# Performance work log

Measured on AMD Instinct MI355X. Metric: run time of the kernel, lower is better.

Reference implementation:

```python
import math
import jax, jax.numpy as jnp
import numpy as np
from jax import lax

N = 224
EPS_BN = 1e-5


def _conv(x, w, b):
    y = lax.conv_general_dilated(x, w, (1, 1), 'SAME',
                                 dimension_numbers=('NCHW', 'OIHW', 'NCHW'))
    return y + b[None, :, None, None]


def _bn(x, g, beta, m, v):
    # eval-mode BatchNorm2d with running stats
    inv = lax.rsqrt(v + EPS_BN)
    return (x - m[None, :, None, None]) * (g * inv)[None, :, None, None] + beta[None, :, None, None]


def _maxpool2(x):
    return lax.reduce_window(x, -jnp.inf, lax.max, (1, 1, 2, 2), (1, 1, 2, 2), 'VALID')


def setup_inputs() -> dict:
    key = jax.random.key(0)
    ks = jax.random.split(key, 12)
    idx = np.arange(N, dtype=np.float32)
    angles = 2.0 * math.pi * idx[None, :] * idx[:, None] / N
    inp = {
        'sequences': jax.random.normal(ks[0], (16, 8, 3, N, N), dtype=jnp.float32),
        'dft_cos': jnp.asarray(np.cos(angles), dtype=jnp.float32),
        'dft_sin': jnp.asarray(np.sin(angles), dtype=jnp.float32),
        'conv1_w': jax.random.normal(ks[1], (16, 3, 3, 3), dtype=jnp.float32) * 0.1,
        'conv1_b': jnp.zeros((16,), jnp.float32),
        'bn1_g': jnp.ones((16,), jnp.float32),
        'bn1_b': jnp.zeros((16,), jnp.float32),
        'bn1_m': jnp.zeros((16,), jnp.float32),
        'bn1_v': jnp.ones((16,), jnp.float32),
        'conv2_w': jax.random.normal(ks[2], (32, 16, 3, 3), dtype=jnp.float32) * 0.05,
        'conv2_b': jnp.zeros((32,), jnp.float32),
        'bn2_g': jnp.ones((32,), jnp.float32),
        'bn2_b': jnp.zeros((32,), jnp.float32),
        'bn2_m': jnp.zeros((32,), jnp.float32),
        'bn2_v': jnp.ones((32,), jnp.float32),
        'conv3_w': jax.random.normal(ks[3], (64, 32, 3, 3), dtype=jnp.float32) * 0.05,
        'conv3_b': jnp.zeros((64,), jnp.float32),
        'bn3_g': jnp.ones((64,), jnp.float32),
        'bn3_b': jnp.zeros((64,), jnp.float32),
        'bn3_m': jnp.zeros((64,), jnp.float32),
        'bn3_v': jnp.ones((64,), jnp.float32),
        'fc_w': jax.random.normal(ks[4], (128, 64), dtype=jnp.float32) * 0.1,
        'fc_b': jnp.zeros((128,), jnp.float32),
    }
    return inp


def reference(sequences, dft_cos, dft_sin,
              conv1_w, conv1_b, bn1_g, bn1_b, bn1_m, bn1_v,
              conv2_w, conv2_b, bn2_g, bn2_b, bn2_m, bn2_v,
              conv3_w, conv3_b, bn3_g, bn3_b, bn3_m, bn3_v,
              fc_w, fc_b):
    b, s = sequences.shape[0], sequences.shape[1]
    x = sequences[:, s // 2]  # center frames [B,3,H,W]

    # 2D DFT via dense matmul chain: X = (C - jS) x (C - jS)
    C, S = dft_cos, dft_sin
    Cx = jnp.einsum('ij,bcjk->bcik', C, x)
    Sx = jnp.einsum('ij,bcjk->bcik', S, x)
    X_real = jnp.einsum('bcij,jk->bcik', Cx, C) - jnp.einsum('bcij,jk->bcik', Sx, S)
    X_imag = -(jnp.einsum('bcij,jk->bcik', Cx, S) + jnp.einsum('bcij,jk->bcik', Sx, C))
    magnitude = jnp.sqrt(X_real ** 2 + X_imag ** 2 + 1e-08)
    spec = jnp.log(magnitude + 1e-08)
    half = N // 2
    spec = jnp.roll(spec, shift=(half, half), axis=(-2, -1))  # fftshift

    # CNN stack (eval-mode BN, dropout disabled)
    h = jax.nn.relu(_bn(_conv(spec, conv1_w, conv1_b), bn1_g, bn1_b, bn1_m, bn1_v))
    h = _maxpool2(h)
    h = jax.nn.relu(_bn(_conv(h, conv2_w, conv2_b), bn2_g, bn2_b, bn2_m, bn2_v))
    h = _maxpool2(h)
    h = jax.nn.relu(_bn(_conv(h, conv3_w, conv3_b), bn3_g, bn3_b, bn3_m, bn3_v))
    h = jnp.mean(h, axis=(2, 3))  # AdaptiveAvgPool2d((1,1)) + flatten -> [B,64]

    freq_out = jax.nn.relu(h @ fc_w.T + fc_b)  # dropout = identity in eval
    return freq_out
```

## Files before the change

kernel.cpp:

```cpp
#include <hip/hip_runtime.h>
#include <math.h>
#include <stddef.h>

#define N224 224
#define PIX 50176
#define ROWS113 25312

__global__ __launch_bounds__(64) void dft1(
    const float* __restrict__ seq, const float* __restrict__ Cm,
    const float* __restrict__ Sm, float* __restrict__ Cx, float* __restrict__ Sx)
{
  const int p = blockIdx.z;
  const int b = p / 3, ch = p % 3;
  const float* __restrict__ x = seq + ((((size_t)b * 8 + 4) * 3 + ch) * PIX);
  const int i0 = blockIdx.y * 32;
  const int k0 = blockIdx.x * 32;
  const int tid = threadIdx.x;
  const int tx = tid & 7, ty = tid >> 3;
  __shared__ float Ctt[16][36], Stt[16][36], Xt[16][36];
  float aC[4][4], aS[4][4];
#pragma unroll
  for (int a = 0; a < 4; ++a)
#pragma unroll
    for (int d = 0; d < 4; ++d) { aC[a][d] = 0.f; aS[a][d] = 0.f; }

  const int sr = tid >> 1;
  const int sk = (tid & 1) * 8;
  const int xj = tid >> 2;
  const int xk = (tid & 3) * 8;

  for (int jt = 0; jt < 14; ++jt) {
    const int j = jt * 16;
    __syncthreads();
    {
      const float4* gp = (const float4*)(x + (size_t)(j + xj) * N224 + k0 + xk);
      const float4 v0 = gp[0], v1 = gp[1];
      *(float4*)&Xt[xj][xk]     = v0;
      *(float4*)&Xt[xj][xk + 4] = v1;
    }
    {
      const float4* gc = (const float4*)(Cm + (size_t)(i0 + sr) * N224 + j + sk);
      const float4* gs = (const float4*)(Sm + (size_t)(i0 + sr) * N224 + j + sk);
      const float4 c0 = gc[0], c1 = gc[1];
      const float4 s0 = gs[0], s1 = gs[1];
      Ctt[sk+0][sr]=c0.x; Ctt[sk+1][sr]=c0.y; Ctt[sk+2][sr]=c0.z; Ctt[sk+3][sr]=c0.w;
      Ctt[sk+4][sr]=c1.x; Ctt[sk+5][sr]=c1.y; Ctt[sk+6][sr]=c1.z; Ctt[sk+7][sr]=c1.w;
      Stt[sk+0][sr]=s0.x; Stt[sk+1][sr]=s0.y; Stt[sk+2][sr]=s0.z; Stt[sk+3][sr]=s0.w;
      Stt[sk+4][sr]=s1.x; Stt[sk+5][sr]=s1.y; Stt[sk+6][sr]=s1.z; Stt[sk+7][sr]=s1.w;
    }
    __syncthreads();
#pragma unroll
    for (int jj = 0; jj < 16; ++jj) {
      const float4 cv4 = *(const float4*)&Ctt[jj][4*ty];
      const float4 sv4 = *(const float4*)&Stt[jj][4*ty];
      const float4 xv4 = *(const float4*)&Xt[jj][4*tx];
      const float cva[4] = {cv4.x, cv4.y, cv4.z, cv4.w};
      const float sva[4] = {sv4.x, sv4.y, sv4.z, sv4.w};
      const float xva[4] = {xv4.x, xv4.y, xv4.z, xv4.w};
#pragma unroll
      for (int a = 0; a < 4; ++a)
#pragma unroll
        for (int d = 0; d < 4; ++d) {
          aC[a][d] = fmaf(cva[a], xva[d], aC[a][d]);
          aS[a][d] = fmaf(sva[a], xva[d], aS[a][d]);
        }
    }
  }
  const size_t b113 = (size_t)p * ROWS113;
#pragma unroll
  for (int a = 0; a < 4; ++a) {
    const int i = i0 + 4*ty + a;
    if (i <= 112) {
      const size_t off = b113 + (size_t)i * N224 + k0 + 4*tx;
      *(float4*)&Cx[off] = make_float4(aC[a][0], aC[a][1], aC[a][2], aC[a][3]);
      *(float4*)&Sx[off] = make_float4(aS[a][0], aS[a][1], aS[a][2], aS[a][3]);
    }
  }
}

__global__ __launch_bounds__(64) void dft2(
    const float* __restrict__ Cx, const float* __restrict__ Sx,
    const float* __restrict__ Cm, const float* __restrict__ Sm,
    float* __restrict__ spec)
{
  const int p = blockIdx.z;
  const int i0 = blockIdx.y * 32;
  const int k0 = blockIdx.x * 32;
  const int tid = threadIdx.x;
  const int tx = tid & 7, ty = tid >> 3;
  const size_t b113 = (size_t)p * ROWS113;
  __shared__ float CxT[16][36], SxT[16][36], Ct[16][36], St[16][36];
  float p1[4][4], p2[4][4], p3[4][4], p4[4][4];
#pragma unroll
  for (int a = 0; a < 4; ++a)
#pragma unroll
    for (int d = 0; d < 4; ++d) { p1[a][d]=0.f; p2[a][d]=0.f; p3[a][d]=0.f; p4[a][d]=0.f; }

  const int sr = tid >> 1;
  const int sk = (tid & 1) * 8;
  const int ri = (i0 + sr > 112) ? 112 : i0 + sr;
  const int xj = tid >> 2;
  const int xk = (tid & 3) * 8;

  for (int jt = 0; jt < 14; ++jt) {
    const int j = jt * 16;
    __syncthreads();
    {
      const float4* gc = (const float4*)(Cm + (size_t)(j + xj) * N224 + k0 + xk);
      const float4* gs = (const float4*)(Sm + (size_t)(j + xj) * N224 + k0 + xk);
      const float4 c0 = gc[0], c1 = gc[1];
      const float4 s0 = gs[0], s1 = gs[1];
      *(float4*)&Ct[xj][xk]     = c0;  *(float4*)&Ct[xj][xk + 4] = c1;
      *(float4*)&St[xj][xk]     = s0;  *(float4*)&St[xj][xk + 4] = s1;
    }
    {
      const float4* gx = (const float4*)(Cx + b113 + (size_t)ri * N224 + j + sk);
      const float4* gy = (const float4*)(Sx + b113 + (size_t)ri * N224 + j + sk);
      const float4 c0 = gx[0], c1 = gx[1];
      const float4 s0 = gy[0], s1 = gy[1];
      CxT[sk+0][sr]=c0.x; CxT[sk+1][sr]=c0.y; CxT[sk+2][sr]=c0.z; CxT[sk+3][sr]=c0.w;
      CxT[sk+4][sr]=c1.x; CxT[sk+5][sr]=c1.y; CxT[sk+6][sr]=c1.z; CxT[sk+7][sr]=c1.w;
      SxT[sk+0][sr]=s0.x; SxT[sk+1][sr]=s0.y; SxT[sk+2][sr]=s0.z; SxT[sk+3][sr]=s0.w;
      SxT[sk+4][sr]=s1.x; SxT[sk+5][sr]=s1.y; SxT[sk+6][sr]=s1.z; SxT[sk+7][sr]=s1.w;
    }
    __syncthreads();
#pragma unroll
    for (int jj = 0; jj < 16; ++jj) {
      const float4 cx4 = *(const float4*)&CxT[jj][4*ty];
      const float4 sx4 = *(const float4*)&SxT[jj][4*ty];
      const float4 cc4 = *(const float4*)&Ct[jj][4*tx];
      const float4 ss4 = *(const float4*)&St[jj][4*tx];
      const float cxa[4] = {cx4.x, cx4.y, cx4.z, cx4.w};
      const float sxa[4] = {sx4.x, sx4.y, sx4.z, sx4.w};
      const float cca[4] = {cc4.x, cc4.y, cc4.z, cc4.w};
      const float ssa[4] = {ss4.x, ss4.y, ss4.z, ss4.w};
#pragma unroll
      for (int a = 0; a < 4; ++a)
#pragma unroll
        for (int d = 0; d < 4; ++d) {
          p1[a][d] = fmaf(cxa[a], cca[d], p1[a][d]);
          p2[a][d] = fmaf(sxa[a], ssa[d], p2[a][d]);
          p3[a][d] = fmaf(cxa[a], ssa[d], p3[a][d]);
          p4[a][d] = fmaf(sxa[a], cca[d], p4[a][d]);
        }
    }
  }
  const size_t sb = (size_t)p * PIX;
  const int kk0 = k0 + 4*tx;
  const int ok0 = (kk0 < 112) ? kk0 + 112 : kk0 - 112;
#pragma unroll
  for (int a = 0; a < 4; ++a) {
    const int i = i0 + 4*ty + a;
    if (i > 112) continue;
    float sp1[4], sp2[4];
#pragma unroll
    for (int d = 0; d < 4; ++d) {
      const float re = p1[a][d] - p2[a][d];
      const float im = p3[a][d] + p4[a][d];
      sp1[d] = logf(sqrtf(fmaf(re, re, fmaf(im, im, 1e-8f))) + 1e-8f);
      const float re2 = p1[a][d] + p2[a][d];
      const float im2 = p3[a][d] - p4[a][d];
      sp2[d] = logf(sqrtf(fmaf(re2, re2, fmaf(im2, im2, 1e-8f))) + 1e-8f);
    }
    const int oi = (i < 112) ? i + 112 : i - 112;
    *(float4*)&spec[sb + (size_t)oi * N224 + ok0] =
        make_float4(sp1[0], sp1[1], sp1[2], sp1[3]);
    if (i >= 1 && i <= 111)
      *(float4*)&spec[sb + (size_t)(112 - i) * N224 + ok0] =
          make_float4(sp2[0], sp2[1], sp2[2], sp2[3]);
  }
}

__global__ __launch_bounds__(256) void conv1_band(
    const float* __restrict__ spec, const float* __restrict__ w,
    const float* __restrict__ cb, const float* __restrict__ g,
    const float* __restrict__ be, const float* __restrict__ mm,
    const float* __restrict__ vv, float* __restrict__ out)
{
  const int band = blockIdx.x;
  const int b    = blockIdx.y;
  const int tid  = threadIdx.x;
  const int co   = tid & 15;
  const int q    = tid >> 4;
  const int cy0  = band * 4;
  __shared__ float in_t[3][6][228];
  __shared__ float wt[3][9][16];
  for (int i = tid; i < 3*6*224; i += 256) {
    const int x = i % 224, r = (i / 224) % 6, cc = i / 1344;
    const int y = cy0 - 1 + r;
    float v = 0.f;
    if (y >= 0 && y < 224)
      v = spec[((size_t)b*3 + cc) * PIX + (size_t)y * N224 + x];
    in_t[cc][r][x+1] = v;
  }
  if (tid < 18) { const int cc = tid / 6, r = tid % 6;
                  in_t[cc][r][0] = 0.f; in_t[cc][r][225] = 0.f; }
  for (int i = tid; i < 3*9*16; i += 256) {
    const int coi = i & 15, k = (i >> 4) % 9, cc = i / 144;
    wt[cc][k][coi] = w[coi*27 + cc*9 + k];
  }
  __syncthreads();
  float acc[4][14];
#pragma unroll
  for (int i = 0; i < 4; ++i)
#pragma unroll
    for (int jx = 0; jx < 14; ++jx) acc[i][jx] = 0.f;
  const int x0 = q * 14;
#pragma unroll
  for (int cc = 0; cc < 3; ++cc) {
    float wr[9];
#pragma unroll
    for (int k = 0; k < 9; ++k) wr[k] = wt[cc][k][co];
#pragma unroll
    for (int rr = 0; rr < 6; ++rr) {
      float xr[16];
      const float2* rp = (const float2*)(&in_t[cc][rr][x0]);
#pragma unroll
      for (int t = 0; t < 8; ++t) { const float2 v = rp[t]; xr[2*t] = v.x; xr[2*t+1] = v.y; }
#pragma unroll
      for (int crow = 0; crow < 4; ++crow) {
        const int krow = rr - crow;
        if (krow < 0 || krow > 2) continue;
#pragma unroll
        for (int xx = 0; xx < 14; ++xx) {
          acc[crow][xx] = fmaf(xr[xx  ], wr[krow*3  ], acc[crow][xx]);
          acc[crow][xx] = fmaf(xr[xx+1], wr[krow*3+1], acc[crow][xx]);
          acc[crow][xx] = fmaf(xr[xx+2], wr[krow*3+2], acc[crow][xx]);
        }
      }
    }
  }
  const float s  = g[co] * rsqrtf(vv[co] + 1e-5f);
  const float sh = be[co] - mm[co]*s;
  const float bb = cb[co];
  const int py0 = band * 2, px0 = q * 7;
#pragma unroll
  for (int pr = 0; pr < 2; ++pr)
#pragma unroll
    for (int px = 0; px < 7; ++px) {
      const float v0 = (acc[2*pr  ][2*px  ] + bb)*s + sh;
      const float v1 = (acc[2*pr  ][2*px+1] + bb)*s + sh;
      const float v2 = (acc[2*pr+1][2*px  ] + bb)*s + sh;
      const float v3 = (acc[2*pr+1][2*px+1] + bb)*s + sh;
      out[(((size_t)b*16 + co)*112 + py0+pr)*112 + px0+px] =
          fmaxf(fmaxf(fmaxf(v0, v1), fmaxf(v2, v3)), 0.f);
    }
}

__global__ __launch_bounds__(256) void conv2_band(
    const float* __restrict__ h1, const float* __restrict__ w,
    const float* __restrict__ cb, const float* __restrict__ g,
    const float* __restrict__ be, const float* __restrict__ mm,
    const float* __restrict__ vv, float* __restrict__ out)
{
  const int band = blockIdx.x;
  const int b    = blockIdx.y;
  const int tid  = threadIdx.x;
  const int co   = tid & 31;
  const int q    = tid >> 5;
  const int cy0  = band * 4;
  __shared__ float in_t[8][6][114];
  __shared__ float wt[8][9][32];
  float acc[4][14];
#pragma unroll
  for (int i = 0; i < 4; ++i)
#pragma unroll
    for (int jx = 0; jx < 14; ++jx) acc[i][jx] = 0.f;

  for (int chunk = 0; chunk < 2; ++chunk) {
    const int ci0 = chunk * 8;
    __syncthreads();
    for (int i = tid; i < 8*6*112; i += 256) {
      const int x = i % 112, r = (i / 112) % 6, cc = i / 672;
      const int y = cy0 - 1 + r;
      float v = 0.f;
      if (y >= 0 && y < 112)
        v = h1[(((size_t)b*16 + ci0+cc)*112 + y)*112 + x];
      in_t[cc][r][x+1] = v;
    }
    if (tid < 48) { const int cc = tid / 6, r = tid % 6;
                    in_t[cc][r][0] = 0.f; in_t[cc][r][113] = 0.f; }
    for (int i = tid; i < 8*9*32; i += 256) {
      const int coi = i & 31, k = (i >> 5) % 9, cc = i / 288;
      wt[cc][k][coi] = w[coi*144 + (ci0+cc)*9 + k];
    }
    __syncthreads();
    const int x0 = q * 14;
    for (int cc = 0; cc < 8; ++cc) {
      float wr[9];
#pragma unroll
      for (int k = 0; k < 9; ++k) wr[k] = wt[cc][k][co];
#pragma unroll
      for (int rr = 0; rr < 6; ++rr) {
        float xr[16];
        const float2* rp = (const float2*)(&in_t[cc][rr][x0]);
#pragma unroll
        for (int t = 0; t < 8; ++t) { const float2 v = rp[t]; xr[2*t] = v.x; xr[2*t+1] = v.y; }
#pragma unroll
        for (int crow = 0; crow < 4; ++crow) {
          const int krow = rr - crow;
          if (krow < 0 || krow > 2) continue;
#pragma unroll
          for (int x = 0; x < 14; ++x) {
            acc[crow][x] = fmaf(xr[x  ], wr[krow*3  ], acc[crow][x]);
            acc[crow][x] = fmaf(xr[x+1], wr[krow*3+1], acc[crow][x]);
            acc[crow][x] = fmaf(xr[x+2], wr[krow*3+2], acc[crow][x]);
          }
        }
      }
    }
  }
  const float s  = g[co] * rsqrtf(vv[co] + 1e-5f);
  const float sh = be[co] - mm[co]*s;
  const float bb = cb[co];
  const int py0 = band * 2, px0 = q * 7;
#pragma unroll
  for (int pr = 0; pr < 2; ++pr)
#pragma unroll
    for (int px = 0; px < 7; ++px) {
      const float v0 = (acc[2*pr  ][2*px  ] + bb)*s + sh;
      const float v1 = (acc[2*pr  ][2*px+1] + bb)*s + sh;
      const float v2 = (acc[2*pr+1][2*px  ] + bb)*s + sh;
      const float v3 = (acc[2*pr+1][2*px+1] + bb)*s + sh;
      out[(((size_t)b*32 + co)*56 + py0+pr)*56 + px0+px] =
          fmaxf(fmaxf(fmaxf(v0, v1), fmaxf(v2, v3)), 0.f);
    }
}

__global__ __launch_bounds__(256) void conv3_band(
    const float* __restrict__ h2, const float* __restrict__ w,
    const float* __restrict__ cb, const float* __restrict__ g,
    const float* __restrict__ be, const float* __restrict__ mm,
    const float* __restrict__ vv, float* __restrict__ part)
{
  const int band = blockIdx.x;
  const int b    = blockIdx.y;
  const int tid  = threadIdx.x;
  const int co   = tid & 63;
  const int q    = tid >> 6;
  const int y0   = band * 2;
  __shared__ float in_t[8][4][58];
  __shared__ float wt[8][9][64];
  __shared__ float red[4][64];
  float acc[2][14];
#pragma unroll
  for (int i = 0; i < 2; ++i)
#pragma unroll
    for (int jx = 0; jx < 14; ++jx) acc[i][jx] = 0.f;

  for (int chunk = 0; chunk < 4; ++chunk) {
    const int ci0 = chunk * 8;
    __syncthreads();
    for (int i = tid; i < 8*4*56; i += 256) {
      const int x = i % 56, r = (i / 56) % 4, cc = i / 224;
      const int y = y0 - 1 + r;
      float v = 0.f;
      if (y >= 0 && y < 56)
        v = h2[(((size_t)b*32 + ci0+cc)*56 + y)*56 + x];
      in_t[cc][r][x+1] = v;
    }
    if (tid < 32) { const int cc = tid >> 2, r = tid & 3;
                    in_t[cc][r][0] = 0.f; in_t[cc][r][57] = 0.f; }
    for (int i = tid; i < 8*9*64; i += 256) {
      const int coi = i & 63, k = (i >> 6) % 9, cc = i / 576;
      wt[cc][k][coi] = w[coi*288 + (ci0+cc)*9 + k];
    }
    __syncthreads();
    const int x0 = q * 14;
    for (int cc = 0; cc < 8; ++cc) {
      float wr[9];
#pragma unroll
      for (int k = 0; k < 9; ++k) wr[k] = wt[cc][k][co];
#pragma unroll
      for (int rr = 0; rr < 4; ++rr) {
        float xr[16];
        const float2* rp = (const float2*)(&in_t[cc][rr][x0]);
#pragma unroll
        for (int t = 0; t < 8; ++t) { const float2 v = rp[t]; xr[2*t] = v.x; xr[2*t+1] = v.y; }
#pragma unroll
        for (int orow = 0; orow < 2; ++orow) {
          const int krow = rr - orow;
          if (krow < 0 || krow > 2) continue;
#pragma unroll
          for (int x = 0; x < 14; ++x) {
            acc[orow][x] = fmaf(xr[x  ], wr[krow*3  ], acc[orow][x]);
            acc[orow][x] = fmaf(xr[x+1], wr[krow*3+1], acc[orow][x]);
            acc[orow][x] = fmaf(xr[x+2], wr[krow*3+2], acc[orow][x]);
          }
        }
      }
    }
  }
  const float s  = g[co] * rsqrtf(vv[co] + 1e-5f);
  const float sh = be[co] - mm[co]*s;
  const float bb = cb[co];
  float sum = 0.f;
#pragma unroll
  for (int orow = 0; orow < 2; ++orow)
#pragma unroll
    for (int x = 0; x < 14; ++x)
      sum += fmaxf((acc[orow][x] + bb)*s + sh, 0.f);
  red[q][co] = sum;
  __syncthreads();
  if (tid < 64)
    part[(((size_t)b*64 + co)*28) + band] =
        red[0][co] + red[1][co] + red[2][co] + red[3][co];
}

__global__ __launch_bounds__(256) void reduce_mean(
    const float* __restrict__ part, float* __restrict__ h3)
{
  const int idx = blockIdx.x * 256 + threadIdx.x;
  if (idx >= 1024) return;
  float s = 0.f;
#pragma unroll
  for (int bnd = 0; bnd < 28; ++bnd) s += part[(size_t)idx*28 + bnd];
  h3[idx] = s * (1.0f / 3136.0f);
}

__global__ __launch_bounds__(256) void fc_relu(
    const float* __restrict__ h3, const float* __restrict__ fw,
    const float* __restrict__ fb, float* __restrict__ out)
{
  const int idx = blockIdx.x * 256 + threadIdx.x;
  if (idx >= 16*128) return;
  const int o = idx % 128, b = idx / 128;
  float acc = fb[o];
#pragma unroll
  for (int c = 0; c < 64; ++c)
    acc = fmaf(h3[b*64 + c], fw[o*64 + c], acc);
  out[idx] = fmaxf(acc, 0.f);
}

extern "C" void kernel_launch(void* const* d_in, const int* in_sizes, int n_in,
                              void* d_out, int out_size, void* d_ws, size_t ws_size,
                              hipStream_t stream) {
  const float* seq  = (const float*)d_in[0];
  const float* dcos = (const float*)d_in[1];
  const float* dsin = (const float*)d_in[2];
  const float* c1w  = (const float*)d_in[3];
  const float* c1b  = (const float*)d_in[4];
  const float* b1g  = (const float*)d_in[5];
  const float* b1b  = (const float*)d_in[6];
  const float* b1m  = (const float*)d_in[7];
  const float* b1v  = (const float*)d_in[8];
  const float* c2w  = (const float*)d_in[9];
  const float* c2b  = (const float*)d_in[10];
  const float* b2g  = (const float*)d_in[11];
  const float* b2b  = (const float*)d_in[12];
  const float* b2m  = (const float*)d_in[13];
  const float* b2v  = (const float*)d_in[14];
  const float* c3w  = (const float*)d_in[15];
  const float* c3b  = (const float*)d_in[16];
  const float* b3g  = (const float*)d_in[17];
  const float* b3b  = (const float*)d_in[18];
  const float* b3m  = (const float*)d_in[19];
  const float* b3v  = (const float*)d_in[20];
  const float* fw   = (const float*)d_in[21];
  const float* fb   = (const float*)d_in[22];
  float* out = (float*)d_out;

  float* ws   = (float*)d_ws;
  float* Cx   = ws;
  float* Sx   = ws + 1214976;
  float* spec = ws + 4816896;
  float* h1   = ws;
  float* h2   = ws + 4816896;
  float* part = ws;
  float* h3   = ws + 7225344;

  dft1<<<dim3(7, 4, 48), 64, 0, stream>>>(seq, dcos, dsin, Cx, Sx);
  dft2<<<dim3(7, 4, 48), 64, 0, stream>>>(Cx, Sx, dcos, dsin, spec);
  conv1_band<<<dim3(56, 16), 256, 0, stream>>>(spec, c1w, c1b, b1g, b1b, b1m, b1v, h1);
  conv2_band<<<dim3(28, 16), 256, 0, stream>>>(h1, c2w, c2b, b2g, b2b, b2m, b2v, h2);
  conv3_band<<<dim3(28, 16), 256, 0, stream>>>(h2, c3w, c3b, b3g, b3b, b3m, b3v, part);
  reduce_mean<<<4, 256, 0, stream>>>(part, h3);
  fc_relu<<<8, 256, 0, stream>>>(h3, fw, fb, out);
}
```

Baseline: 197.9 us.

## Prefetch DFT tiles into registers, halve conv bands, fuse mean and FC

The two DFT matmul kernels now load the next k-tile from global memory into registers while the current tile is being computed, a register-level double buffer that hides load latency. Each conv kernel now handles half as many rows per block, so twice as many blocks are launched to fill the GPU better. In exchange, the overlapping halo rows are reloaded more often. The reduce-mean and FC kernels are merged into a single kernel, removing one launch.

```diff
diff --git a/kernel.cpp b/kernel.cpp
--- a/kernel.cpp
+++ b/kernel.cpp
@@ -29,26 +29,35 @@
   const int xj = tid >> 2;
   const int xk = (tid & 3) * 8;
 
+  const float* xbase = x  + (size_t)xj * N224 + k0 + xk;
+  const float* cbase = Cm + (size_t)(i0 + sr) * N224 + sk;
+  const float* sbase = Sm + (size_t)(i0 + sr) * N224 + sk;
+
+  float4 rx0 = *(const float4*)(xbase);
+  float4 rx1 = *(const float4*)(xbase + 4);
+  float4 rc0 = *(const float4*)(cbase);
+  float4 rc1 = *(const float4*)(cbase + 4);
+  float4 rs0 = *(const float4*)(sbase);
+  float4 rs1 = *(const float4*)(sbase + 4);
+
   for (int jt = 0; jt < 14; ++jt) {
-    const int j = jt * 16;
-    __syncthreads();
-    {
-      const float4* gp = (const float4*)(x + (size_t)(j + xj) * N224 + k0 + xk);
-      const float4 v0 = gp[0], v1 = gp[1];
-      *(float4*)&Xt[xj][xk]     = v0;
-      *(float4*)&Xt[xj][xk + 4] = v1;
-    }
-    {
-      const float4* gc = (const float4*)(Cm + (size_t)(i0 + sr) * N224 + j + sk);
-      const float4* gs = (const float4*)(Sm + (size_t)(i0 + sr) * N224 + j + sk);
-      const float4 c0 = gc[0], c1 = gc[1];
-      const float4 s0 = gs[0], s1 = gs[1];
-      Ctt[sk+0][sr]=c0.x; Ctt[sk+1][sr]=c0.y; Ctt[sk+2][sr]=c0.z; Ctt[sk+3][sr]=c0.w;
-      Ctt[sk+4][sr]=c1.x; Ctt[sk+5][sr]=c1.y; Ctt[sk+6][sr]=c1.z; Ctt[sk+7][sr]=c1.w;
-      Stt[sk+0][sr]=s0.x; Stt[sk+1][sr]=s0.y; Stt[sk+2][sr]=s0.z; Stt[sk+3][sr]=s0.w;
-      Stt[sk+4][sr]=s1.x; Stt[sk+5][sr]=s1.y; Stt[sk+6][sr]=s1.z; Stt[sk+7][sr]=s1.w;
-    }
-    __syncthreads();
+    __syncthreads();
+    *(float4*)&Xt[xj][xk]     = rx0;
+    *(float4*)&Xt[xj][xk + 4] = rx1;
+    Ctt[sk+0][sr]=rc0.x; Ctt[sk+1][sr]=rc0.y; Ctt[sk+2][sr]=rc0.z; Ctt[sk+3][sr]=rc0.w;
+    Ctt[sk+4][sr]=rc1.x; Ctt[sk+5][sr]=rc1.y; Ctt[sk+6][sr]=rc1.z; Ctt[sk+7][sr]=rc1.w;
+    Stt[sk+0][sr]=rs0.x; Stt[sk+1][sr]=rs0.y; Stt[sk+2][sr]=rs0.z; Stt[sk+3][sr]=rs0.w;
+    Stt[sk+4][sr]=rs1.x; Stt[sk+5][sr]=rs1.y; Stt[sk+6][sr]=rs1.z; Stt[sk+7][sr]=rs1.w;
+    __syncthreads();
+    if (jt < 13) {
+      const int j = (jt + 1) * 16;
+      rx0 = *(const float4*)(xbase + (size_t)j * N224);
+      rx1 = *(const float4*)(xbase + (size_t)j * N224 + 4);
+      rc0 = *(const float4*)(cbase + j);
+      rc1 = *(const float4*)(cbase + j + 4);
+      rs0 = *(const float4*)(sbase + j);
+      rs1 = *(const float4*)(sbase + j + 4);
+    }
 #pragma unroll
     for (int jj = 0; jj < 16; ++jj) {
       const float4 cv4 = *(const float4*)&Ctt[jj][4*ty];
@@ -102,28 +111,40 @@
   const int xj = tid >> 2;
   const int xk = (tid & 3) * 8;
 
+  const float* cxb = Cx + b113 + (size_t)ri * N224 + sk;
+  const float* sxb = Sx + b113 + (size_t)ri * N224 + sk;
+  const float* ccb = Cm + (size_t)xj * N224 + k0 + xk;
+  const float* ssb = Sm + (size_t)xj * N224 + k0 + xk;
+
+  float4 ra0 = *(const float4*)(cxb);
+  float4 ra1 = *(const float4*)(cxb + 4);
+  float4 rb0 = *(const float4*)(sxb);
+  float4 rb1 = *(const float4*)(sxb + 4);
+  float4 rc0 = *(const float4*)(ccb);
+  float4 rc1 = *(const float4*)(ccb + 4);
+  float4 rd0 = *(const float4*)(ssb);
+  float4 rd1 = *(const float4*)(ssb + 4);
+
   for (int jt = 0; jt < 14; ++jt) {
-    const int j = jt * 16;
-    __syncthreads();
-    {
-      const float4* gc = (const float4*)(Cm + (size_t)(j + xj) * N224 + k0 + xk);
-      const float4* gs = (const float4*)(Sm + (size_t)(j + xj) * N224 + k0 + xk);
-      const float4 c0 = gc[0], c1 = gc[1];
-      const float4 s0 = gs[0], s1 = gs[1];
-      *(float4*)&Ct[xj][xk]     = c0;  *(float4*)&Ct[xj][xk + 4] = c1;
-      *(float4*)&St[xj][xk]     = s0;  *(float4*)&St[xj][xk + 4] = s1;
-    }
-    {
-      const float4* gx = (const float4*)(Cx + b113 + (size_t)ri * N224 + j + sk);
-      const float4* gy = (const float4*)(Sx + b113 + (size_t)ri * N224 + j + sk);
-      const float4 c0 = gx[0], c1 = gx[1];
-      const float4 s0 = gy[0], s1 = gy[1];
-      CxT[sk+0][sr]=c0.x; CxT[sk+1][sr]=c0.y; CxT[sk+2][sr]=c0.z; CxT[sk+3][sr]=c0.w;
-      CxT[sk+4][sr]=c1.x; CxT[sk+5][sr]=c1.y; CxT[sk+6][sr]=c1.z; CxT[sk+7][sr]=c1.w;
-      SxT[sk+0][sr]=s0.x; SxT[sk+1][sr]=s0.y; SxT[sk+2][sr]=s0.z; SxT[sk+3][sr]=s0.w;
-      SxT[sk+4][sr]=s1.x; SxT[sk+5][sr]=s1.y; SxT[sk+6][sr]=s1.z; SxT[sk+7][sr]=s1.w;
-    }
-    __syncthreads();
+    __syncthreads();
+    *(float4*)&Ct[xj][xk]     = rc0;  *(float4*)&Ct[xj][xk + 4] = rc1;
+    *(float4*)&St[xj][xk]     = rd0;  *(float4*)&St[xj][xk + 4] = rd1;
+    CxT[sk+0][sr]=ra0.x; CxT[sk+1][sr]=ra0.y; CxT[sk+2][sr]=ra0.z; CxT[sk+3][sr]=ra0.w;
+    CxT[sk+4][sr]=ra1.x; CxT[sk+5][sr]=ra1.y; CxT[sk+6][sr]=ra1.z; CxT[sk+7][sr]=ra1.w;
+    SxT[sk+0][sr]=rb0.x; SxT[sk+1][sr]=rb0.y; SxT[sk+2][sr]=rb0.z; SxT[sk+3][sr]=rb0.w;
+    SxT[sk+4][sr]=rb1.x; SxT[sk+5][sr]=rb1.y; SxT[sk+6][sr]=rb1.z; SxT[sk+7][sr]=rb1.w;
+    __syncthreads();
+    if (jt < 13) {
+      const int j = (jt + 1) * 16;
+      ra0 = *(const float4*)(cxb + j);
+      ra1 = *(const float4*)(cxb + j + 4);
+      rb0 = *(const float4*)(sxb + j);
+      rb1 = *(const float4*)(sxb + j + 4);
+      rc0 = *(const float4*)(ccb + (size_t)j * N224);
+      rc1 = *(const float4*)(ccb + (size_t)j * N224 + 4);
+      rd0 = *(const float4*)(ssb + (size_t)j * N224);
+      rd1 = *(const float4*)(ssb + (size_t)j * N224 + 4);
+    }
 #pragma unroll
     for (int jj = 0; jj < 16; ++jj) {
       const float4 cx4 = *(const float4*)&CxT[jj][4*ty];
@@ -182,27 +203,27 @@
   const int tid  = threadIdx.x;
   const int co   = tid & 15;
   const int q    = tid >> 4;
-  const int cy0  = band * 4;
-  __shared__ float in_t[3][6][228];
+  const int cy0  = band * 2;
+  __shared__ float in_t[3][4][228];
   __shared__ float wt[3][9][16];
-  for (int i = tid; i < 3*6*224; i += 256) {
-    const int x = i % 224, r = (i / 224) % 6, cc = i / 1344;
+  for (int i = tid; i < 3*4*224; i += 256) {
+    const int x = i % 224, r = (i / 224) % 4, cc = i / 896;
     const int y = cy0 - 1 + r;
     float v = 0.f;
     if (y >= 0 && y < 224)
       v = spec[((size_t)b*3 + cc) * PIX + (size_t)y * N224 + x];
     in_t[cc][r][x+1] = v;
   }
-  if (tid < 18) { const int cc = tid / 6, r = tid % 6;
+  if (tid < 12) { const int cc = tid / 4, r = tid % 4;
                   in_t[cc][r][0] = 0.f; in_t[cc][r][225] = 0.f; }
   for (int i = tid; i < 3*9*16; i += 256) {
     const int coi = i & 15, k = (i >> 4) % 9, cc = i / 144;
     wt[cc][k][coi] = w[coi*27 + cc*9 + k];
   }
   __syncthreads();
-  float acc[4][14];
-#pragma unroll
-  for (int i = 0; i < 4; ++i)
+  float acc[2][14];
+#pragma unroll
+  for (int i = 0; i < 2; ++i)
 #pragma unroll
     for (int jx = 0; jx < 14; ++jx) acc[i][jx] = 0.f;
   const int x0 = q * 14;
@@ -212,13 +233,13 @@
 #pragma unroll
     for (int k = 0; k < 9; ++k) wr[k] = wt[cc][k][co];
 #pragma unroll
-    for (int rr = 0; rr < 6; ++rr) {
+    for (int rr = 0; rr < 4; ++rr) {
       float xr[16];
       const float2* rp = (const float2*)(&in_t[cc][rr][x0]);
 #pragma unroll
       for (int t = 0; t < 8; ++t) { const float2 v = rp[t]; xr[2*t] = v.x; xr[2*t+1] = v.y; }
 #pragma unroll
-      for (int crow = 0; crow < 4; ++crow) {
+      for (int crow = 0; crow < 2; ++crow) {
         const int krow = rr - crow;
         if (krow < 0 || krow > 2) continue;
 #pragma unroll
@@ -233,18 +254,16 @@
   const float s  = g[co] * rsqrtf(vv[co] + 1e-5f);
   const float sh = be[co] - mm[co]*s;
   const float bb = cb[co];
-  const int py0 = band * 2, px0 = q * 7;
-#pragma unroll
-  for (int pr = 0; pr < 2; ++pr)
-#pragma unroll
-    for (int px = 0; px < 7; ++px) {
-      const float v0 = (acc[2*pr  ][2*px  ] + bb)*s + sh;
-      const float v1 = (acc[2*pr  ][2*px+1] + bb)*s + sh;
-      const float v2 = (acc[2*pr+1][2*px  ] + bb)*s + sh;
-      const float v3 = (acc[2*pr+1][2*px+1] + bb)*s + sh;
-      out[(((size_t)b*16 + co)*112 + py0+pr)*112 + px0+px] =
-          fmaxf(fmaxf(fmaxf(v0, v1), fmaxf(v2, v3)), 0.f);
-    }
+  const int px0 = q * 7;
+#pragma unroll
+  for (int px = 0; px < 7; ++px) {
+    const float v0 = (acc[0][2*px  ] + bb)*s + sh;
+    const float v1 = (acc[0][2*px+1] + bb)*s + sh;
+    const float v2 = (acc[1][2*px  ] + bb)*s + sh;
+    const float v3 = (acc[1][2*px+1] + bb)*s + sh;
+    out[(((size_t)b*16 + co)*112 + band)*112 + px0+px] =
+        fmaxf(fmaxf(fmaxf(v0, v1), fmaxf(v2, v3)), 0.f);
+  }
 }
 
 __global__ __launch_bounds__(256) void conv2_band(
@@ -258,27 +277,27 @@
   const int tid  = threadIdx.x;
   const int co   = tid & 31;
   const int q    = tid >> 5;
-  const int cy0  = band * 4;
-  __shared__ float in_t[8][6][114];
+  const int cy0  = band * 2;
+  __shared__ float in_t[8][4][114];
   __shared__ float wt[8][9][32];
-  float acc[4][14];
-#pragma unroll
-  for (int i = 0; i < 4; ++i)
+  float acc[2][14];
+#pragma unroll
+  for (int i = 0; i < 2; ++i)
 #pragma unroll
     for (int jx = 0; jx < 14; ++jx) acc[i][jx] = 0.f;
 
   for (int chunk = 0; chunk < 2; ++chunk) {
     const int ci0 = chunk * 8;
     __syncthreads();
-    for (int i = tid; i < 8*6*112; i += 256) {
-      const int x = i % 112, r = (i / 112) % 6, cc = i / 672;
+    for (int i = tid; i < 8*4*112; i += 256) {
+      const int x = i % 112, r = (i / 112) % 4, cc = i / 448;
       const int y = cy0 - 1 + r;
       float v = 0.f;
       if (y >= 0 && y < 112)
         v = h1[(((size_t)b*16 + ci0+cc)*112 + y)*112 + x];
       in_t[cc][r][x+1] = v;
     }
-    if (tid < 48) { const int cc = tid / 6, r = tid % 6;
+    if (tid < 32) { const int cc = tid >> 2, r = tid & 3;
                     in_t[cc][r][0] = 0.f; in_t[cc][r][113] = 0.f; }
     for (int i = tid; i < 8*9*32; i += 256) {
       const int coi = i & 31, k = (i >> 5) % 9, cc = i / 288;
@@ -291,13 +310,13 @@
 #pragma unroll
       for (int k = 0; k < 9; ++k) wr[k] = wt[cc][k][co];
 #pragma unroll
-      for (int rr = 0; rr < 6; ++rr) {
+      for (int rr = 0; rr < 4; ++rr) {
         float xr[16];
         const float2* rp = (const float2*)(&in_t[cc][rr][x0]);
 #pragma unroll
         for (int t = 0; t < 8; ++t) { const float2 v = rp[t]; xr[2*t] = v.x; xr[2*t+1] = v.y; }
 #pragma unroll
-        for (int crow = 0; crow < 4; ++crow) {
+        for (int crow = 0; crow < 2; ++crow) {
           const int krow = rr - crow;
           if (krow < 0 || krow > 2) continue;
 #pragma unroll
@@ -313,18 +332,16 @@
   const float s  = g[co] * rsqrtf(vv[co] + 1e-5f);
   const float sh = be[co] - mm[co]*s;
   const float bb = cb[co];
-  const int py0 = band * 2, px0 = q * 7;
-#pragma unroll
-  for (int pr = 0; pr < 2; ++pr)
-#pragma unroll
-    for (int px = 0; px < 7; ++px) {
-      const float v0 = (acc[2*pr  ][2*px  ] + bb)*s + sh;
-      const float v1 = (acc[2*pr  ][2*px+1] + bb)*s + sh;
-      const float v2 = (acc[2*pr+1][2*px  ] + bb)*s + sh;
-      const float v3 = (acc[2*pr+1][2*px+1] + bb)*s + sh;
-      out[(((size_t)b*32 + co)*56 + py0+pr)*56 + px0+px] =
-          fmaxf(fmaxf(fmaxf(v0, v1), fmaxf(v2, v3)), 0.f);
-    }
+  const int px0 = q * 7;
+#pragma unroll
+  for (int px = 0; px < 7; ++px) {
+    const float v0 = (acc[0][2*px  ] + bb)*s + sh;
+    const float v1 = (acc[0][2*px+1] + bb)*s + sh;
+    const float v2 = (acc[1][2*px  ] + bb)*s + sh;
+    const float v3 = (acc[1][2*px+1] + bb)*s + sh;
+    out[(((size_t)b*32 + co)*56 + band)*56 + px0+px] =
+        fmaxf(fmaxf(fmaxf(v0, v1), fmaxf(v2, v3)), 0.f);
+  }
 }
 
 __global__ __launch_bounds__(256) void conv3_band(
@@ -338,28 +355,26 @@
   const int tid  = threadIdx.x;
   const int co   = tid & 63;
   const int q    = tid >> 6;
-  const int y0   = band * 2;
-  __shared__ float in_t[8][4][58];
+  const int y0   = band;
+  __shared__ float in_t[8][3][58];
   __shared__ float wt[8][9][64];
   __shared__ float red[4][64];
-  float acc[2][14];
-#pragma unroll
-  for (int i = 0; i < 2; ++i)
-#pragma unroll
-    for (int jx = 0; jx < 14; ++jx) acc[i][jx] = 0.f;
+  float acc[14];
+#pragma unroll
+  for (int jx = 0; jx < 14; ++jx) acc[jx] = 0.f;
 
   for (int chunk = 0; chunk < 4; ++chunk) {
     const int ci0 = chunk * 8;
     __syncthreads();
-    for (int i = tid; i < 8*4*56; i += 256) {
-      const int x = i % 56, r = (i / 56) % 4, cc = i / 224;
+    for (int i = tid; i < 8*3*56; i += 256) {
+      const int x = i % 56, r = (i / 56) % 3, cc = i / 168;
       const int y = y0 - 1 + r;
       float v = 0.f;
       if (y >= 0 && y < 56)
         v = h2[(((size_t)b*32 + ci0+cc)*56 + y)*56 + x];
       in_t[cc][r][x+1] = v;
     }
-    if (tid < 32) { const int cc = tid >> 2, r = tid & 3;
+    if (tid < 24) { const int cc = tid / 3, r = tid % 3;
                     in_t[cc][r][0] = 0.f; in_t[cc][r][57] = 0.f; }
     for (int i = tid; i < 8*9*64; i += 256) {
       const int coi = i & 63, k = (i >> 6) % 9, cc = i / 576;
@@ -372,21 +387,16 @@
 #pragma unroll
       for (int k = 0; k < 9; ++k) wr[k] = wt[cc][k][co];
 #pragma unroll
-      for (int rr = 0; rr < 4; ++rr) {
+      for (int rr = 0; rr < 3; ++rr) {
         float xr[16];
         const float2* rp = (const float2*)(&in_t[cc][rr][x0]);
 #pragma unroll
         for (int t = 0; t < 8; ++t) { const float2 v = rp[t]; xr[2*t] = v.x; xr[2*t+1] = v.y; }
 #pragma unroll
-        for (int orow = 0; orow < 2; ++orow) {
-          const int krow = rr - orow;
-          if (krow < 0 || krow > 2) continue;
-#pragma unroll
-          for (int x = 0; x < 14; ++x) {
-            acc[orow][x] = fmaf(xr[x  ], wr[krow*3  ], acc[orow][x]);
-            acc[orow][x] = fmaf(xr[x+1], wr[krow*3+1], acc[orow][x]);
-            acc[orow][x] = fmaf(xr[x+2], wr[krow*3+2], acc[orow][x]);
-          }
+        for (int x = 0; x < 14; ++x) {
+          acc[x] = fmaf(xr[x  ], wr[rr*3  ], acc[x]);
+          acc[x] = fmaf(xr[x+1], wr[rr*3+1], acc[x]);
+          acc[x] = fmaf(xr[x+2], wr[rr*3+2], acc[x]);
         }
       }
     }
@@ -396,40 +406,35 @@
   const float bb = cb[co];
   float sum = 0.f;
 #pragma unroll
-  for (int orow = 0; orow < 2; ++orow)
-#pragma unroll
-    for (int x = 0; x < 14; ++x)
-      sum += fmaxf((acc[orow][x] + bb)*s + sh, 0.f);
+  for (int x = 0; x < 14; ++x)
+    sum += fmaxf((acc[x] + bb)*s + sh, 0.f);
   red[q][co] = sum;
   __syncthreads();
   if (tid < 64)
-    part[(((size_t)b*64 + co)*28) + band] =
+    part[(((size_t)b*64 + co)*56) + band] =
         red[0][co] + red[1][co] + red[2][co] + red[3][co];
 }
 
-__global__ __launch_bounds__(256) void reduce_mean(
-    const float* __restrict__ part, float* __restrict__ h3)
-{
-  const int idx = blockIdx.x * 256 + threadIdx.x;
-  if (idx >= 1024) return;
-  float s = 0.f;
-#pragma unroll
-  for (int bnd = 0; bnd < 28; ++bnd) s += part[(size_t)idx*28 + bnd];
-  h3[idx] = s * (1.0f / 3136.0f);
-}
-
-__global__ __launch_bounds__(256) void fc_relu(
-    const float* __restrict__ h3, const float* __restrict__ fw,
+__global__ __launch_bounds__(128) void mean_fc(
+    const float* __restrict__ part, const float* __restrict__ fw,
     const float* __restrict__ fb, float* __restrict__ out)
 {
-  const int idx = blockIdx.x * 256 + threadIdx.x;
-  if (idx >= 16*128) return;
-  const int o = idx % 128, b = idx / 128;
-  float acc = fb[o];
+  const int b = blockIdx.x;
+  const int tid = threadIdx.x;
+  __shared__ float h3s[64];
+  if (tid < 64) {
+    float s = 0.f;
+    const float* pp = part + ((size_t)b*64 + tid)*56;
+#pragma unroll
+    for (int i = 0; i < 56; ++i) s += pp[i];
+    h3s[tid] = s * (1.0f / 3136.0f);
+  }
+  __syncthreads();
+  float acc = fb[tid];
 #pragma unroll
   for (int c = 0; c < 64; ++c)
-    acc = fmaf(h3[b*64 + c], fw[o*64 + c], acc);
-  out[idx] = fmaxf(acc, 0.f);
+    acc = fmaf(h3s[c], fw[tid*64 + c], acc);
+  out[b*128 + tid] = fmaxf(acc, 0.f);
 }
 
 extern "C" void kernel_launch(void* const* d_in, const int* in_sizes, int n_in,
@@ -467,13 +472,11 @@
   float* h1   = ws;
   float* h2   = ws + 4816896;
   float* part = ws;
-  float* h3   = ws + 7225344;
 
   dft1<<<dim3(7, 4, 48), 64, 0, stream>>>(seq, dcos, dsin, Cx, Sx);
   dft2<<<dim3(7, 4, 48), 64, 0, stream>>>(Cx, Sx, dcos, dsin, spec);
-  conv1_band<<<dim3(56, 16), 256, 0, stream>>>(spec, c1w, c1b, b1g, b1b, b1m, b1v, h1);
-  conv2_band<<<dim3(28, 16), 256, 0, stream>>>(h1, c2w, c2b, b2g, b2b, b2m, b2v, h2);
-  conv3_band<<<dim3(28, 16), 256, 0, stream>>>(h2, c3w, c3b, b3g, b3b, b3m, b3v, part);
-  reduce_mean<<<4, 256, 0, stream>>>(part, h3);
-  fc_relu<<<8, 256, 0, stream>>>(h3, fw, fb, out);
-}
+  conv1_band<<<dim3(112, 16), 256, 0, stream>>>(spec, c1w, c1b, b1g, b1b, b1m, b1v, h1);
+  conv2_band<<<dim3(56, 16), 256, 0, stream>>>(h1, c2w, c2b, b2g, b2b, b2m, b2v, h2);
+  conv3_band<<<dim3(56, 16), 256, 0, stream>>>(h2, c3w, c3b, b3g, b3b, b3m, b3v, part);
+  mean_fc<<<16, 128, 0, stream>>>(part, fw, fb, out);
+}
```

Measured after the change: 197.7 us. About the same (-0.1%).
